# Optimization experiments

Hardware: AMD Instinct MI355X
Metric: run time of the kernel (lower is better)

## Reference

```python
import jax, jax.numpy as jnp
import numpy as np

A, B, O, C = 8, 32768, 256, 64   # num_agents, batch, obs_size, action_size
E, H = 128, 4                     # embedding_dim, attention_heads
Dh = E // H                       # attend_dim = 32
EPS = 1e-5                        # BatchNorm1d eps
SLOPE = 0.01                      # LeakyReLU default negative slope


def lrelu(x):
    return jnp.where(x >= 0, x, SLOPE * x)


def batchnorm(x, gamma, beta):
    # x: [A,B,F]; training-mode BatchNorm1d per agent (biased batch variance)
    mu = x.mean(axis=1, keepdims=True)
    var = x.var(axis=1, keepdims=True)
    return (x - mu) / jnp.sqrt(var + EPS) * gamma[:, None, :] + beta[:, None, :]


def setup_inputs() -> dict:
    key = jax.random.key(0)
    ks = jax.random.split(key, 13)
    s = lambda k, shape: jax.random.normal(k, shape, jnp.float32) * 0.05
    return {
        "observation_vector": jax.random.normal(ks[0], (A, B, O), jnp.float32),
        "action_vector": jax.random.normal(ks[1], (A, B, C), jnp.float32),
        "g_bn_gamma": jnp.ones((A, O + C), jnp.float32),
        "g_bn_beta": jnp.zeros((A, O + C), jnp.float32),
        "g_W": s(ks[2], (A, E, O + C)), "g_b": s(ks[3], (A, E)),
        "s_bn_gamma": jnp.ones((A, O), jnp.float32),
        "s_bn_beta": jnp.zeros((A, O), jnp.float32),
        "s_W": s(ks[4], (A, E, O)), "s_b": s(ks[5], (A, E)),
        "f_W1": s(ks[6], (A, E, 2 * E)), "f_b1": s(ks[7], (A, E)),
        "f_W2": s(ks[8], (A, C, E)), "f_b2": s(ks[9], (A, C)),
        "Wq": s(ks[10], (H, Dh, E)), "Wk": s(ks[11], (H, Dh, E)),
        "V": s(ks[12], (H, Dh, E)),
    }


def reference(observation_vector, action_vector, g_bn_gamma, g_bn_beta, g_W, g_b,
              s_bn_gamma, s_bn_beta, s_W, s_b, f_W1, f_b1, f_W2, f_b2, Wq, Wk, V):
    # per-agent embeddings of (obs, act) and obs-only
    combined = jnp.concatenate([observation_vector, action_vector], axis=2)      # [A,B,O+C]
    e = lrelu(jnp.einsum('abf,aef->abe', batchnorm(combined, g_bn_gamma, g_bn_beta), g_W)
              + g_b[:, None, :])                                                  # [A,B,E]
    si = lrelu(jnp.einsum('abf,aef->abe',
                          batchnorm(observation_vector, s_bn_gamma, s_bn_beta), s_W)
               + s_b[:, None, :])                                                 # [A,B,E]
    # NOTE: original applies F.softmax over a (batch,1) tensor -> every attention
    # weight is exactly 1.0, so x_i = sum_{j!=i} leaky_relu(V_l @ e_j). Wq/Wk only
    # feed the regularization logits (not returned when regularize=False).
    v = lrelu(jnp.einsum('abe,hde->abhd', e, V))                                  # [A,B,H,Dh]
    x = (v.sum(axis=0, keepdims=True) - v).reshape(A, B, E)                       # heads concatenated
    h = lrelu(jnp.einsum('abf,aef->abe', jnp.concatenate([x, si], axis=2), f_W1)
              + f_b1[:, None, :])                                                 # [A,B,E]
    q_all = jnp.einsum('abe,ace->abc', h, f_W2) + f_b2[:, None, :]                # [A,B,C]
    ids = jnp.argmax(action_vector, axis=2)[..., None]                            # [A,B,1]
    return jnp.take_along_axis(q_all, ids, axis=2)                                # [A,B,1]
```

## Files before the change

kernel.cpp:

```cpp
#include <hip/hip_runtime.h>
#include <hip/hip_bf16.h>
#include <stdint.h>

constexpr int A_ = 8, B_ = 32768, O_ = 256, C_ = 64, F_ = 320, E_ = 128;
constexpr int NCH = 128, CHROWS = B_ / NCH;
constexpr int NBT = B_ / 16;

typedef __attribute__((ext_vector_type(8))) __bf16 bf16x8;
typedef __attribute__((ext_vector_type(4))) float f32x4;
union U4 { uint4 u; bf16x8 v; __bf16 b[8]; };

__device__ __forceinline__ float lrelu(float x){ return x >= 0.f ? x : 0.01f*x; }
__device__ __forceinline__ f32x4 mfma16(bf16x8 a, bf16x8 b, f32x4 c){
  return __builtin_amdgcn_mfma_f32_16x16x32_bf16(a, b, c, 0, 0, 0);
}
__device__ __forceinline__ bf16x8 pk8(f32x4 lo, f32x4 hi){
  U4 r;
  r.b[0]=(__bf16)lo[0]; r.b[1]=(__bf16)lo[1]; r.b[2]=(__bf16)lo[2]; r.b[3]=(__bf16)lo[3];
  r.b[4]=(__bf16)hi[0]; r.b[5]=(__bf16)hi[1]; r.b[6]=(__bf16)hi[2]; r.b[7]=(__bf16)hi[3];
  return r.v;
}
__device__ __forceinline__ bf16x8 pk8f(float4 a, float4 b){
  U4 r;
  r.b[0]=(__bf16)a.x; r.b[1]=(__bf16)a.y; r.b[2]=(__bf16)a.z; r.b[3]=(__bf16)a.w;
  r.b[4]=(__bf16)b.x; r.b[5]=(__bf16)b.y; r.b[6]=(__bf16)b.z; r.b[7]=(__bf16)b.w;
  return r.v;
}
__device__ __forceinline__ void gl_lds16(const void* g, void* s){
  __builtin_amdgcn_global_load_lds(
      (const __attribute__((address_space(1))) unsigned int*)g,
      (__attribute__((address_space(3))) unsigned int*)s, 16, 0, 0);
}
template<int N> __device__ __forceinline__ void vmwait(){
  asm volatile("s_waitcnt vmcnt(%0)" :: "n"(N) : "memory");
}
__device__ __forceinline__ void lgkm0(){ asm volatile("s_waitcnt lgkmcnt(0)" ::: "memory"); }
__device__ __forceinline__ void sbar(){ __builtin_amdgcn_s_barrier(); }
__device__ __forceinline__ void schb(){ __builtin_amdgcn_sched_barrier(0); }

__global__ void k_stats_partial(const float* __restrict__ obs,
                                const float* __restrict__ act,
                                float* __restrict__ psum, float* __restrict__ psq,
                                int* __restrict__ ids){
  const int f = threadIdx.x, ch = blockIdx.x, a = blockIdx.y;
  const size_t b0 = (size_t)ch * CHROWS;
  float s = 0.f, q = 0.f;
  if (f < O_){
    const float* p = obs + ((size_t)a*B_ + b0)*O_ + f;
    for (int i = 0; i < CHROWS; ++i){ float x = p[(size_t)i*O_]; s += x; q += x*x; }
  } else {
    const float* p = act + ((size_t)a*B_ + b0)*C_ + (f - O_);
    for (int i = 0; i < CHROWS; ++i){ float x = p[(size_t)i*C_]; s += x; q += x*x; }
  }
  psum[((size_t)a*NCH + ch)*F_ + f] = s;
  psq [((size_t)a*NCH + ch)*F_ + f] = q;
  if (f < CHROWS){
    const float4* ar = (const float4*)(act + ((size_t)a*B_ + b0 + f)*C_);
    float best = -3.4e38f; int bi = 0;
    #pragma unroll 4
    for (int j = 0; j < 16; ++j){
      const float4 v = ar[j];
      const int c0 = j*4;
      if (v.x > best){ best = v.x; bi = c0;   }
      if (v.y > best){ best = v.y; bi = c0+1; }
      if (v.z > best){ best = v.z; bi = c0+2; }
      if (v.w > best){ best = v.w; bi = c0+3; }
    }
    ids[(size_t)a*B_ + b0 + f] = bi;
  }
}

__global__ void k_stats_final(const float* __restrict__ psum, const float* __restrict__ psq,
                              float* __restrict__ zscale, float* __restrict__ zshift){
  const int f = threadIdx.x, a = blockIdx.x;
  float s = 0.f, q = 0.f;
  for (int ch = 0; ch < NCH; ++ch){
    s += psum[((size_t)a*NCH + ch)*F_ + f];
    q += psq [((size_t)a*NCH + ch)*F_ + f];
  }
  const float mean = s * (1.0f / B_);
  float var = q * (1.0f / B_) - mean * mean;
  var = fmaxf(var, 0.0f);
  const float rs = rsqrtf(var + 1e-5f);
  zscale[a*F_ + f] = rs;
  zshift[a*F_ + f] = -mean * rs;
}

__global__ void k_prep_pack(const float* __restrict__ gW, const float* __restrict__ ggam,
                            const float* __restrict__ sW, const float* __restrict__ sgam,
                            const float* __restrict__ f1W, const float* __restrict__ f2W,
                            const float* __restrict__ Vm, const float* __restrict__ zscale,
                            __bf16* __restrict__ Ap, __bf16* __restrict__ Vp,
                            __bf16* __restrict__ B1p, __bf16* __restrict__ B2p){
  const int a = blockIdx.y;
  const int t0 = blockIdx.x*256 + threadIdx.x;
  constexpr int STR = 32*256;
  for (int i = t0; i < 10*16*64*8; i += STR){
    const int ks = i >> 13, mO = (i>>9)&15, l = (i>>3)&63, e = i&7;
    const int lg = l>>4, fo = mO*16 + (l&15), k = ks*32 + lg*8 + e;
    const float sc = zscale[a*F_ + k];
    float v;
    if (fo < 128) v = gW[(size_t)a*E_*F_ + (size_t)fo*F_ + k] * ggam[a*F_+k] * sc;
    else          v = (k < O_) ? sW[(size_t)a*E_*O_ + (size_t)(fo-128)*O_ + k] * sgam[a*O_+k] * sc : 0.f;
    Ap[(size_t)a*(10*16*64*8) + i] = (__bf16)v;
  }
  for (int i = t0; i < 8*8*64*8; i += STR){
    const int ks = i >> 12, mH = (i>>9)&7, l = (i>>3)&63, e = i&7;
    const int lg = l>>4, h = mH*16 + (l&15);
    const int f = 32*ks + 16*(e>>2) + 4*lg + (e&3);
    B1p[(size_t)a*(8*8*64*8) + i] = (__bf16)f1W[(size_t)a*E_*2*E_ + (size_t)h*2*E_ + f];
  }
  for (int i = t0; i < 4*4*64*8; i += STR){
    const int ks = i >> 11, mC = (i>>9)&3, l = (i>>3)&63, e = i&7;
    const int lg = l>>4, c = mC*16 + (l&15);
    const int f = 32*ks + 16*(e>>2) + 4*lg + (e&3);
    B2p[(size_t)a*(4*4*64*8) + i] = (__bf16)f2W[(size_t)a*C_*E_ + (size_t)c*E_ + f];
  }
  if (a == 0){
    for (int i = t0; i < 4*8*64*8; i += STR){
      const int ks = i >> 12, mV = (i>>9)&7, l = (i>>3)&63, e = i&7;
      const int lg = l>>4, vo = mV*16 + (l&15);
      const int f = 32*ks + 16*(e>>2) + 4*lg + (e&3);
      Vp[i] = (__bf16)Vm[(size_t)vo*E_ + f];
    }
  }
}

__global__ void k_prep_bias(const float* __restrict__ gW, const float* __restrict__ gb,
                            const float* __restrict__ ggam, const float* __restrict__ gbet,
                            const float* __restrict__ sW, const float* __restrict__ sb,
                            const float* __restrict__ sgam, const float* __restrict__ sbet,
                            const float* __restrict__ zshift, float* __restrict__ gsb){
  __shared__ float ww[F_];
  __shared__ float part[2][128];
  const int a = blockIdx.y, t = threadIdx.x;
  const int o = t & 127, h = t >> 7;
  if (blockIdx.x == 0){
    for (int f = t; f < F_; f += 256)
      ww[f] = gbet[a*F_+f] + ggam[a*F_+f]*zshift[a*F_+f];
    __syncthreads();
    float s = 0.f;
    #pragma unroll 4
    for (int f = h*160; f < h*160 + 160; f += 4){
      const float4 wv = *(const float4*)&gW[(size_t)a*E_*F_ + (size_t)o*F_ + f];
      s += wv.x*ww[f] + wv.y*ww[f+1] + wv.z*ww[f+2] + wv.w*ww[f+3];
    }
    part[h][o] = s;
    __syncthreads();
    if (t < 128) gsb[a*256 + t] = gb[a*E_+t] + part[0][t] + part[1][t];
  } else {
    for (int f = t; f < O_; f += 256)
      ww[f] = sbet[a*O_+f] + sgam[a*O_+f]*zshift[a*F_+f];
    __syncthreads();
    float s = 0.f;
    #pragma unroll 4
    for (int f = h*128; f < h*128 + 128; f += 4){
      const float4 wv = *(const float4*)&sW[(size_t)a*E_*O_ + (size_t)o*O_ + f];
      s += wv.x*ww[f] + wv.y*ww[f+1] + wv.z*ww[f+2] + wv.w*ww[f+3];
    }
    part[h][o] = s;
    __syncthreads();
    if (t < 128) gsb[a*256 + 128 + t] = sb[a*E_+t] + part[0][t] + part[1][t];
  }
}

__global__ __launch_bounds__(256, 2) void k_stageA(
    const float* __restrict__ obs, const float* __restrict__ act,
    const __bf16* __restrict__ Ap, const __bf16* __restrict__ Vp,
    const float* __restrict__ gsb,
    uint4* __restrict__ si_q, uint4* __restrict__ v_q){
  constexpr int BUF = 26624;
  __shared__ __align__(16) char smem[2*BUF];
  const int a = blockIdx.y, t = threadIdx.x;
  const int w = t>>6, l = t&63, l15 = l&15, lg = l>>4;
  const int bt0 = blockIdx.x*8;
  const size_t grow0 = (size_t)a*B_ + (size_t)bt0*16;
  const char* ApA = (const char*)Ap + (size_t)a*163840;
  const int xr = t>>1, kc0 = (t&1)*2;
  const float* obsrow = obs + (grow0 + xr)*O_;
  const float* actrow = act + (grow0 + xr)*C_;

  float4 xA[4], xB[4];

  auto wstage = [&](int ks, char* buf){
    const char* src = ApA + ks*16384;
    #pragma unroll
    for (int i = 0; i < 4; ++i)
      gl_lds16(src + (w*4+i)*1024 + l*16, buf + (w*4+i)*1024);
  };
  auto xload = [&](int ks, float4* d){
    const float* s = (ks < 8) ? (obsrow + ks*32 + kc0*8) : (actrow + (ks-8)*32 + kc0*8);
    d[0] = ((const float4*)s)[0]; d[1] = ((const float4*)s)[1];
    d[2] = ((const float4*)s)[2]; d[3] = ((const float4*)s)[3];
  };
  auto xwrite = [&](char* buf, const float4* d){
    *(bf16x8*)(buf + 16384 + xr*80 + kc0*16)     = pk8f(d[0], d[1]);
    *(bf16x8*)(buf + 16384 + xr*80 + (kc0+1)*16) = pk8f(d[2], d[3]);
  };

  f32x4 acc[4][8] = {};

  wstage(0, smem); schb();
  xload(0, xA);
  vmwait<0>();
  xwrite(smem, xA);
  xload(1, xB);
  lgkm0(); sbar(); schb();

  #pragma unroll
  for (int ks = 0; ks < 10; ++ks){
    char* cur = smem + (ks&1)*BUF;
    char* nxt = smem + ((ks+1)&1)*BUF;
    if (ks+1 < 10){ wstage(ks+1, nxt); schb(); }
    if (ks+2 < 10) xload(ks+2, (ks&1) ? xB : xA);
    {
      const bf16x8* wc = (const bf16x8*)cur;
      const char* xb = cur + 16384;
      bf16x8 bfr[8];
      #pragma unroll
      for (int nt = 0; nt < 8; ++nt)
        bfr[nt] = *(const bf16x8*)(xb + (nt*16 + l15)*80 + lg*16);
      #pragma unroll
      for (int m = 0; m < 4; ++m){
        const bf16x8 af = wc[(w*4+m)*64 + l];
        #pragma unroll
        for (int nt = 0; nt < 8; ++nt)
          acc[m][nt] = mfma16(af, bfr[nt], acc[m][nt]);
      }
    }
    schb();
    if (ks <= 7)      vmwait<4>();
    else if (ks == 8) vmwait<0>();
    if (ks+1 < 10) xwrite(nxt, (ks&1) ? xA : xB);
    if (ks < 9){ lgkm0(); sbar(); schb(); }
  }

  const float* bE = gsb + a*256 + w*64 + lg*4;
  #pragma unroll
  for (int m = 0; m < 4; ++m){
    const float4 b = *(const float4*)(bE + m*16);
    #pragma unroll
    for (int nt = 0; nt < 8; ++nt){
      acc[m][nt][0] = lrelu(acc[m][nt][0] + b.x);
      acc[m][nt][1] = lrelu(acc[m][nt][1] + b.y);
      acc[m][nt][2] = lrelu(acc[m][nt][2] + b.z);
      acc[m][nt][3] = lrelu(acc[m][nt][3] + b.w);
    }
  }
  sbar();

  if (w < 2){
    #pragma unroll
    for (int jp = 0; jp < 2; ++jp){
      const int kv = 2*w + jp;
      #pragma unroll
      for (int nt = 0; nt < 8; ++nt)
        *(bf16x8*)(smem + ((kv*8 + nt)*64 + l)*16) = pk8(acc[2*jp][nt], acc[2*jp+1][nt]);
    }
  } else {
    #pragma unroll
    for (int jp = 0; jp < 2; ++jp){
      const int j = 2*(w-2) + jp;
      #pragma unroll
      for (int nt = 0; nt < 8; ++nt){
        U4 u; u.v = pk8(acc[2*jp][nt], acc[2*jp+1][nt]);
        si_q[(((size_t)a*NBT + bt0 + nt)*4 + j)*64 + l] = u.u;
      }
    }
  }
  lgkm0(); sbar(); schb();

  const uint4* Vq = (const uint4*)Vp;
  f32x4 accv[2][8] = {};
  #pragma unroll
  for (int kv = 0; kv < 4; ++kv){
    U4 a0, a1;
    a0.u = Vq[(kv*8 + w*2 + 0)*64 + l];
    a1.u = Vq[(kv*8 + w*2 + 1)*64 + l];
    bf16x8 bv[8];
    #pragma unroll
    for (int nt = 0; nt < 8; ++nt)
      bv[nt] = *(const bf16x8*)(smem + ((kv*8 + nt)*64 + l)*16);
    #pragma unroll
    for (int nt = 0; nt < 8; ++nt){
      accv[0][nt] = mfma16(a0.v, bv[nt], accv[0][nt]);
      accv[1][nt] = mfma16(a1.v, bv[nt], accv[1][nt]);
    }
  }
  #pragma unroll
  for (int nt = 0; nt < 8; ++nt){
    f32x4 lo, hi;
    #pragma unroll
    for (int e = 0; e < 4; ++e){ lo[e] = lrelu(accv[0][nt][e]); hi[e] = lrelu(accv[1][nt][e]); }
    U4 u; u.v = pk8(lo, hi);
    v_q[(((size_t)a*NBT + bt0 + nt)*4 + w)*64 + l] = u.u;
  }
}

__global__ void k_vsum(const uint4* __restrict__ v_q, uint4* __restrict__ vsum_q){
  const size_t i = (size_t)blockIdx.x*256 + threadIdx.x;
  const size_t per_a = (size_t)NBT*4*64;
  float s[8] = {0,0,0,0,0,0,0,0};
  #pragma unroll
  for (int aa = 0; aa < 8; ++aa){
    U4 u; u.u = v_q[aa*per_a + i];
    #pragma unroll
    for (int e = 0; e < 8; ++e) s[e] += (float)u.b[e];
  }
  U4 o;
  #pragma unroll
  for (int e = 0; e < 8; ++e) o.b[e] = (__bf16)s[e];
  vsum_q[i] = o.u;
}

__global__ __launch_bounds__(256, 2) void k_stageC(
    const uint4* __restrict__ v_q, const uint4* __restrict__ si_q,
    const uint4* __restrict__ vsum_q,
    const __bf16* __restrict__ B1p, const __bf16* __restrict__ B2p,
    const float* __restrict__ f1b, const float* __restrict__ f2b,
    const int* __restrict__ ids, float* __restrict__ out){
  __shared__ __align__(16) char wsm[2*8192];
  __shared__ float qs[4][64][17];
  const int a = blockIdx.y, t = threadIdx.x;
  const int w = t>>6, l = t&63, l15 = l&15, lg = l>>4;
  const int btw = blockIdx.x*16 + w*4;
  const char* B1A = (const char*)B1p + (size_t)a*65536;
  const size_t vbase = (size_t)a*NBT*4*64;

  uint4 qA[4], qB[4], sA[4], sB[4];

  auto wstage = [&](int ks, char* dst){
    const char* src = B1A + ks*8192;
    #pragma unroll
    for (int i = 0; i < 2; ++i)
      gl_lds16(src + (w*2+i)*1024 + l*16, dst + (w*2+i)*1024);
  };
  auto bload = [&](int ks, uint4* qv, uint4* sv){
    if (ks < 4){
      #pragma unroll
      for (int nt = 0; nt < 4; ++nt){
        const size_t idx = ((size_t)(btw+nt)*4 + ks)*64 + l;
        qv[nt] = v_q[vbase + idx];
        sv[nt] = vsum_q[idx];
      }
    } else {
      #pragma unroll
      for (int nt = 0; nt < 4; ++nt)
        qv[nt] = si_q[vbase + ((size_t)(btw+nt)*4 + (ks-4))*64 + l];
    }
  };
  auto bmake = [&](int ks, const uint4* qv, const uint4* sv, bf16x8* bf){
    if (ks < 4){
      #pragma unroll
      for (int nt = 0; nt < 4; ++nt){
        U4 s, v; s.u = sv[nt]; v.u = qv[nt];
        f32x4 lo, hi;
        #pragma unroll
        for (int e = 0; e < 4; ++e){
          lo[e] = (float)s.b[e]   - (float)v.b[e];
          hi[e] = (float)s.b[e+4] - (float)v.b[e+4];
        }
        bf[nt] = pk8(lo, hi);
      }
    } else {
      #pragma unroll
      for (int nt = 0; nt < 4; ++nt){ U4 u; u.u = qv[nt]; bf[nt] = u.v; }
    }
  };

  f32x4 hacc[8][4] = {};
  wstage(0, wsm); schb();
  bload(0, qA, sA); schb();
  bload(1, qB, sB);
  vmwait<8>();
  sbar(); schb();

  #pragma unroll
  for (int ks = 0; ks < 8; ++ks){
    bf16x8 bf[4];
    bmake(ks, (ks&1) ? qB : qA, (ks&1) ? sB : sA, bf);
    if (ks+1 < 8){ wstage(ks+1, wsm + ((ks+1)&1)*8192); schb(); }
    if (ks+2 < 8) bload(ks+2, (ks&1) ? qB : qA, (ks&1) ? sB : sA);
    {
      const bf16x8* wc = (const bf16x8*)(wsm + (ks&1)*8192);
      #pragma unroll
      for (int m = 0; m < 8; ++m){
        const bf16x8 af = wc[m*64 + l];
        #pragma unroll
        for (int nt = 0; nt < 4; ++nt)
          hacc[m][nt] = mfma16(af, bf[nt], hacc[m][nt]);
      }
    }
    schb();
    if (ks <= 1)      vmwait<8>();
    else if (ks <= 5) vmwait<4>();
    else if (ks == 6) vmwait<0>();
    if (ks < 7){ sbar(); schb(); }
  }

  bf16x8 hb[4][4];
  const float* bH = f1b + a*E_ + lg*4;
  #pragma unroll
  for (int kq = 0; kq < 4; ++kq){
    const float4 b0v = *(const float4*)(bH + (2*kq)*16);
    const float4 b1v = *(const float4*)(bH + (2*kq+1)*16);
    #pragma unroll
    for (int nt = 0; nt < 4; ++nt){
      f32x4 lo, hi;
      lo[0]=lrelu(hacc[2*kq][nt][0]+b0v.x); lo[1]=lrelu(hacc[2*kq][nt][1]+b0v.y);
      lo[2]=lrelu(hacc[2*kq][nt][2]+b0v.z); lo[3]=lrelu(hacc[2*kq][nt][3]+b0v.w);
      hi[0]=lrelu(hacc[2*kq+1][nt][0]+b1v.x); hi[1]=lrelu(hacc[2*kq+1][nt][1]+b1v.y);
      hi[2]=lrelu(hacc[2*kq+1][nt][2]+b1v.z); hi[3]=lrelu(hacc[2*kq+1][nt][3]+b1v.w);
      hb[kq][nt] = pk8(lo, hi);
    }
  }
  const uint4* A2q = (const uint4*)(B2p + (size_t)a*(4*4*64*8));
  f32x4 accq[4][4] = {};
  #pragma unroll
  for (int kq = 0; kq < 4; ++kq){
    #pragma unroll
    for (int mC = 0; mC < 4; ++mC){
      U4 af; af.u = A2q[(kq*4 + mC)*64 + l];
      #pragma unroll
      for (int nt = 0; nt < 4; ++nt)
        accq[mC][nt] = mfma16(af.v, hb[kq][nt], accq[mC][nt]);
    }
  }
  const float* bQ = f2b + a*C_ + lg*4;
  float4 qb[4];
  #pragma unroll
  for (int mC = 0; mC < 4; ++mC) qb[mC] = *(const float4*)(bQ + mC*16);
  #pragma unroll
  for (int nt = 0; nt < 4; ++nt){
    #pragma unroll
    for (int mC = 0; mC < 4; ++mC){
      qs[w][mC*16 + lg*4 + 0][l15] = accq[mC][nt][0] + qb[mC].x;
      qs[w][mC*16 + lg*4 + 1][l15] = accq[mC][nt][1] + qb[mC].y;
      qs[w][mC*16 + lg*4 + 2][l15] = accq[mC][nt][2] + qb[mC].z;
      qs[w][mC*16 + lg*4 + 3][l15] = accq[mC][nt][3] + qb[mC].w;
    }
    lgkm0();
    if (l < 16){
      const size_t row = (size_t)(btw + nt)*16 + l;
      const int id = ids[(size_t)a*B_ + row];
      out[(size_t)a*B_ + row] = qs[w][id][l];
    }
    lgkm0();
  }
}

extern "C" void kernel_launch(void* const* d_in, const int* in_sizes, int n_in,
                              void* d_out, int out_size, void* d_ws, size_t ws_size,
                              hipStream_t stream) {
  const float* obs  = (const float*)d_in[0];
  const float* act  = (const float*)d_in[1];
  const float* ggam = (const float*)d_in[2];
  const float* gbet = (const float*)d_in[3];
  const float* gW   = (const float*)d_in[4];
  const float* gb   = (const float*)d_in[5];
  const float* sgam = (const float*)d_in[6];
  const float* sbet = (const float*)d_in[7];
  const float* sW   = (const float*)d_in[8];
  const float* sb   = (const float*)d_in[9];
  const float* f1W  = (const float*)d_in[10];
  const float* f1b  = (const float*)d_in[11];
  const float* f2W  = (const float*)d_in[12];
  const float* f2b  = (const float*)d_in[13];
  const float* Vm   = (const float*)d_in[16];
  float* out = (float*)d_out;

  char* base = (char*)d_ws; size_t off = 0;
  auto alloc = [&](size_t bytes) -> void* {
    off = (off + 255) & ~(size_t)255; void* p = base + off; off += bytes; return p;
  };
  float* psum    = (float*)alloc((size_t)A_*NCH*F_*4);
  float* psq     = (float*)alloc((size_t)A_*NCH*F_*4);
  float* zscale  = (float*)alloc((size_t)A_*F_*4);
  float* zshift  = (float*)alloc((size_t)A_*F_*4);
  float* gsb     = (float*)alloc((size_t)A_*256*4);
  __bf16* Ap     = (__bf16*)alloc((size_t)A_*10*16*64*8*2);
  __bf16* Vp     = (__bf16*)alloc((size_t)4*8*64*8*2);
  __bf16* B1p    = (__bf16*)alloc((size_t)A_*8*8*64*8*2);
  __bf16* B2p    = (__bf16*)alloc((size_t)A_*4*4*64*8*2);
  uint4* si_q    = (uint4*)alloc((size_t)A_*NBT*4*64*16);
  uint4* v_q     = (uint4*)alloc((size_t)A_*NBT*4*64*16);
  uint4* vsum_q  = (uint4*)alloc((size_t)NBT*4*64*16);
  int*   ids     = (int*)alloc((size_t)A_*B_*4);
  (void)ws_size; (void)in_sizes; (void)n_in; (void)out_size;

  k_stats_partial<<<dim3(NCH, A_), 320, 0, stream>>>(obs, act, psum, psq, ids);
  k_stats_final<<<A_, F_, 0, stream>>>(psum, psq, zscale, zshift);
  k_prep_pack<<<dim3(32, A_), 256, 0, stream>>>(gW, ggam, sW, sgam, f1W, f2W, Vm,
                                                zscale, Ap, Vp, B1p, B2p);
  k_prep_bias<<<dim3(2, A_), 256, 0, stream>>>(gW, gb, ggam, gbet, sW, sb, sgam, sbet,
                                               zshift, gsb);
  k_stageA<<<dim3(NBT/8, A_), 256, 0, stream>>>(obs, act, Ap, Vp, gsb, si_q, v_q);
  k_vsum<<<(NBT*4*64)/256, 256, 0, stream>>>(v_q, vsum_q);
  k_stageC<<<dim3(NBT/16, A_), 256, 0, stream>>>(v_q, si_q, vsum_q, B1p, B2p,
                                                 f1b, f2b, ids, out);
}
```

Before: 271.1 us.

## Pre-pack inputs to bf16 during stats pass and stream packed tiles into stageA

The statistics kernel now reads obs/act once in row tiles, computes per-column partial sums through shared memory, computes argmax ids, and writes a swizzled bf16 copy of the inputs in MFMA-ready layout. StageA then loads this half-size packed tensor directly into LDS through a three-deep global_load_lds ring. Weights are held in registers, double-buffered. This removes stageA's second fp32 read of the inputs and its in-kernel conversion. The cost is an extra bf16 write and read of the packed activations, plus more partial-sum blocks for the final reduction.

```diff
diff --git a/kernel.cpp b/kernel.cpp
--- a/kernel.cpp
+++ b/kernel.cpp
@@ -3,7 +3,7 @@
 #include <stdint.h>
 
 constexpr int A_ = 8, B_ = 32768, O_ = 256, C_ = 64, F_ = 320, E_ = 128;
-constexpr int NCH = 128, CHROWS = B_ / NCH;
+constexpr int NRB = B_ / 128;
 constexpr int NBT = B_ / 16;
 
 typedef __attribute__((ext_vector_type(8))) __bf16 bf16x8;
@@ -38,35 +38,68 @@
 __device__ __forceinline__ void sbar(){ __builtin_amdgcn_s_barrier(); }
 __device__ __forceinline__ void schb(){ __builtin_amdgcn_sched_barrier(0); }
 
-__global__ void k_stats_partial(const float* __restrict__ obs,
-                                const float* __restrict__ act,
-                                float* __restrict__ psum, float* __restrict__ psq,
-                                int* __restrict__ ids){
-  const int f = threadIdx.x, ch = blockIdx.x, a = blockIdx.y;
-  const size_t b0 = (size_t)ch * CHROWS;
-  float s = 0.f, q = 0.f;
-  if (f < O_){
-    const float* p = obs + ((size_t)a*B_ + b0)*O_ + f;
-    for (int i = 0; i < CHROWS; ++i){ float x = p[(size_t)i*O_]; s += x; q += x*x; }
-  } else {
-    const float* p = act + ((size_t)a*B_ + b0)*C_ + (f - O_);
-    for (int i = 0; i < CHROWS; ++i){ float x = p[(size_t)i*C_]; s += x; q += x*x; }
-  }
-  psum[((size_t)a*NCH + ch)*F_ + f] = s;
-  psq [((size_t)a*NCH + ch)*F_ + f] = q;
-  if (f < CHROWS){
-    const float4* ar = (const float4*)(act + ((size_t)a*B_ + b0 + f)*C_);
-    float best = -3.4e38f; int bi = 0;
+__global__ __launch_bounds__(256) void k_xstats(
+    const float* __restrict__ obs, const float* __restrict__ act,
+    __bf16* __restrict__ xpk, float* __restrict__ psum, float* __restrict__ psq,
+    int* __restrict__ ids){
+  __shared__ float tile[128*36];
+  __shared__ float sred[32][9], qred[32][9];
+  const int a = blockIdx.y, rb = blockIdx.x, t = threadIdx.x;
+  const int r = t >> 1, fh = t & 1;
+  const size_t row0 = (size_t)a*B_ + (size_t)rb*128;
+  float abest = -3.4e38f; int abi = 0;
+
+  for (int c = 0; c < 10; ++c){
+    const float* src = (c < 8) ? obs + (row0 + r)*O_ + c*32 + fh*16
+                               : act + (row0 + r)*C_ + (c-8)*32 + fh*16;
+    const float4 v0 = ((const float4*)src)[0];
+    const float4 v1 = ((const float4*)src)[1];
+    const float4 v2 = ((const float4*)src)[2];
+    const float4 v3 = ((const float4*)src)[3];
+    if (c >= 8){
+      const int fb = (c-8)*32 + fh*16;
+      const float4 vv[4] = {v0, v1, v2, v3};
+      #pragma unroll
+      for (int j = 0; j < 4; ++j){
+        if (vv[j].x > abest){ abest = vv[j].x; abi = fb + j*4;   }
+        if (vv[j].y > abest){ abest = vv[j].y; abi = fb + j*4+1; }
+        if (vv[j].z > abest){ abest = vv[j].z; abi = fb + j*4+2; }
+        if (vv[j].w > abest){ abest = vv[j].w; abi = fb + j*4+3; }
+      }
+    }
+    const int u = r >> 1, swz = u & 7;
+    const int j0 = ((r&1)*4 + fh*2    ) ^ swz;
+    const int j1 = ((r&1)*4 + fh*2 + 1) ^ swz;
+    bf16x8* xb = (bf16x8*)xpk + ((size_t)(a*NRB + rb)*10 + c)*512 + u*8;
+    xb[j0] = pk8f(v0, v1);
+    xb[j1] = pk8f(v2, v3);
+    float* tr = tile + r*36 + fh*16;
+    *(float4*)(tr)    = v0; *(float4*)(tr+4)  = v1;
+    *(float4*)(tr+8)  = v2; *(float4*)(tr+12) = v3;
+    __syncthreads();
+    const int f = t & 31, g = t >> 5;
+    float s = 0.f, q = 0.f;
     #pragma unroll 4
-    for (int j = 0; j < 16; ++j){
-      const float4 v = ar[j];
-      const int c0 = j*4;
-      if (v.x > best){ best = v.x; bi = c0;   }
-      if (v.y > best){ best = v.y; bi = c0+1; }
-      if (v.z > best){ best = v.z; bi = c0+2; }
-      if (v.w > best){ best = v.w; bi = c0+3; }
-    }
-    ids[(size_t)a*B_ + b0 + f] = bi;
+    for (int i = 0; i < 16; ++i){
+      const float x = tile[(g*16+i)*36 + f];
+      s += x; q += x*x;
+    }
+    sred[f][g] = s; qred[f][g] = q;
+    __syncthreads();
+    if (t < 32){
+      float ss = 0.f, qq = 0.f;
+      #pragma unroll
+      for (int g2 = 0; g2 < 8; ++g2){ ss += sred[t][g2]; qq += qred[t][g2]; }
+      psum[((size_t)a*NRB + rb)*F_ + c*32 + t] = ss;
+      psq [((size_t)a*NRB + rb)*F_ + c*32 + t] = qq;
+    }
+    __syncthreads();
+  }
+  {
+    const float ob = __shfl_xor(abest, 1, 64);
+    const int   oi = __shfl_xor(abi,   1, 64);
+    if (ob > abest || (ob == abest && oi < abi)){ abest = ob; abi = oi; }
+    if (fh == 0) ids[row0 + r] = abi;
   }
 }
 
@@ -74,9 +107,9 @@
                               float* __restrict__ zscale, float* __restrict__ zshift){
   const int f = threadIdx.x, a = blockIdx.x;
   float s = 0.f, q = 0.f;
-  for (int ch = 0; ch < NCH; ++ch){
-    s += psum[((size_t)a*NCH + ch)*F_ + f];
-    q += psq [((size_t)a*NCH + ch)*F_ + f];
+  for (int rb = 0; rb < NRB; ++rb){
+    s += psum[((size_t)a*NRB + rb)*F_ + f];
+    q += psq [((size_t)a*NRB + rb)*F_ + f];
   }
   const float mean = s * (1.0f / B_);
   float var = q * (1.0f / B_) - mean * mean;
@@ -164,75 +197,59 @@
   }
 }
 
-__global__ __launch_bounds__(256, 2) void k_stageA(
-    const float* __restrict__ obs, const float* __restrict__ act,
+__global__ __launch_bounds__(256) void k_stageA(
+    const __bf16* __restrict__ xpk,
     const __bf16* __restrict__ Ap, const __bf16* __restrict__ Vp,
     const float* __restrict__ gsb,
     uint4* __restrict__ si_q, uint4* __restrict__ v_q){
-  constexpr int BUF = 26624;
-  __shared__ __align__(16) char smem[2*BUF];
+  __shared__ __align__(16) char smem[32768];
   const int a = blockIdx.y, t = threadIdx.x;
   const int w = t>>6, l = t&63, l15 = l&15, lg = l>>4;
-  const int bt0 = blockIdx.x*8;
-  const size_t grow0 = (size_t)a*B_ + (size_t)bt0*16;
+  const int rb = blockIdx.x;
+  const int bt0 = rb*8;
+  const char* xT  = (const char*)xpk + ((size_t)(a*NRB + rb))*81920;
   const char* ApA = (const char*)Ap + (size_t)a*163840;
-  const int xr = t>>1, kc0 = (t&1)*2;
-  const float* obsrow = obs + (grow0 + xr)*O_;
-  const float* actrow = act + (grow0 + xr)*C_;
-
-  float4 xA[4], xB[4];
-
-  auto wstage = [&](int ks, char* buf){
-    const char* src = ApA + ks*16384;
-    #pragma unroll
-    for (int i = 0; i < 4; ++i)
-      gl_lds16(src + (w*4+i)*1024 + l*16, buf + (w*4+i)*1024);
+  const int xcj = (((l15&1)<<2) | lg) ^ ((l15>>1)&7);
+  const int xbase = (l15>>1)*128 + xcj*16;
+
+  U4 wA[2][4];
+  auto wload = [&](int ks){
+    const uint4* p = (const uint4*)(ApA + ks*16384) + w*256 + l;
+    U4* d = wA[ks&1];
+    d[0].u = p[0]; d[1].u = p[64]; d[2].u = p[128]; d[3].u = p[192];
   };
-  auto xload = [&](int ks, float4* d){
-    const float* s = (ks < 8) ? (obsrow + ks*32 + kc0*8) : (actrow + (ks-8)*32 + kc0*8);
-    d[0] = ((const float4*)s)[0]; d[1] = ((const float4*)s)[1];
-    d[2] = ((const float4*)s)[2]; d[3] = ((const float4*)s)[3];
+  auto xstage = [&](int ks){
+    const char* s = xT + ks*8192;
+    char* d = smem + (ks%3)*8192;
+    gl_lds16(s + ((w*2+0)*64+l)*16, d + (w*2+0)*1024);
+    gl_lds16(s + ((w*2+1)*64+l)*16, d + (w*2+1)*1024);
   };
-  auto xwrite = [&](char* buf, const float4* d){
-    *(bf16x8*)(buf + 16384 + xr*80 + kc0*16)     = pk8f(d[0], d[1]);
-    *(bf16x8*)(buf + 16384 + xr*80 + (kc0+1)*16) = pk8f(d[2], d[3]);
-  };
 
   f32x4 acc[4][8] = {};
-
-  wstage(0, smem); schb();
-  xload(0, xA);
-  vmwait<0>();
-  xwrite(smem, xA);
-  xload(1, xB);
-  lgkm0(); sbar(); schb();
+  wload(0); schb();
+  xstage(0); xstage(1); schb();
+  vmwait<2>(); sbar(); schb();
 
   #pragma unroll
   for (int ks = 0; ks < 10; ++ks){
-    char* cur = smem + (ks&1)*BUF;
-    char* nxt = smem + ((ks+1)&1)*BUF;
-    if (ks+1 < 10){ wstage(ks+1, nxt); schb(); }
-    if (ks+2 < 10) xload(ks+2, (ks&1) ? xB : xA);
-    {
-      const bf16x8* wc = (const bf16x8*)cur;
-      const char* xb = cur + 16384;
-      bf16x8 bfr[8];
+    if (ks+1 < 10){ wload(ks+1); schb(); }
+    if (ks+2 < 10){ xstage(ks+2); schb(); }
+    const char* xb = smem + (ks%3)*8192;
+    bf16x8 bfr[8];
+    #pragma unroll
+    for (int nt = 0; nt < 8; ++nt)
+      bfr[nt] = *(const bf16x8*)(xb + nt*1024 + xbase);
+    #pragma unroll
+    for (int m = 0; m < 4; ++m){
+      const bf16x8 af = wA[ks&1][m].v;
       #pragma unroll
       for (int nt = 0; nt < 8; ++nt)
-        bfr[nt] = *(const bf16x8*)(xb + (nt*16 + l15)*80 + lg*16);
-      #pragma unroll
-      for (int m = 0; m < 4; ++m){
-        const bf16x8 af = wc[(w*4+m)*64 + l];
-        #pragma unroll
-        for (int nt = 0; nt < 8; ++nt)
-          acc[m][nt] = mfma16(af, bfr[nt], acc[m][nt]);
-      }
+        acc[m][nt] = mfma16(af, bfr[nt], acc[m][nt]);
     }
     schb();
-    if (ks <= 7)      vmwait<4>();
+    if (ks < 8)       vmwait<2>();
     else if (ks == 8) vmwait<0>();
-    if (ks+1 < 10) xwrite(nxt, (ks&1) ? xA : xB);
-    if (ks < 9){ lgkm0(); sbar(); schb(); }
+    if (ks < 9){ sbar(); schb(); }
   }
 
   const float* bE = gsb + a*256 + w*64 + lg*4;
@@ -473,11 +490,12 @@
   auto alloc = [&](size_t bytes) -> void* {
     off = (off + 255) & ~(size_t)255; void* p = base + off; off += bytes; return p;
   };
-  float* psum    = (float*)alloc((size_t)A_*NCH*F_*4);
-  float* psq     = (float*)alloc((size_t)A_*NCH*F_*4);
+  float* psum    = (float*)alloc((size_t)A_*NRB*F_*4);
+  float* psq     = (float*)alloc((size_t)A_*NRB*F_*4);
   float* zscale  = (float*)alloc((size_t)A_*F_*4);
   float* zshift  = (float*)alloc((size_t)A_*F_*4);
   float* gsb     = (float*)alloc((size_t)A_*256*4);
+  __bf16* xpk    = (__bf16*)alloc((size_t)A_*NRB*10*512*16);
   __bf16* Ap     = (__bf16*)alloc((size_t)A_*10*16*64*8*2);
   __bf16* Vp     = (__bf16*)alloc((size_t)4*8*64*8*2);
   __bf16* B1p    = (__bf16*)alloc((size_t)A_*8*8*64*8*2);
@@ -488,13 +506,13 @@
   int*   ids     = (int*)alloc((size_t)A_*B_*4);
   (void)ws_size; (void)in_sizes; (void)n_in; (void)out_size;
 
-  k_stats_partial<<<dim3(NCH, A_), 320, 0, stream>>>(obs, act, psum, psq, ids);
+  k_xstats<<<dim3(NRB, A_), 256, 0, stream>>>(obs, act, xpk, psum, psq, ids);
   k_stats_final<<<A_, F_, 0, stream>>>(psum, psq, zscale, zshift);
   k_prep_pack<<<dim3(32, A_), 256, 0, stream>>>(gW, ggam, sW, sgam, f1W, f2W, Vm,
                                                 zscale, Ap, Vp, B1p, B2p);
   k_prep_bias<<<dim3(2, A_), 256, 0, stream>>>(gW, gb, ggam, gbet, sW, sb, sgam, sbet,
                                                zshift, gsb);
-  k_stageA<<<dim3(NBT/8, A_), 256, 0, stream>>>(obs, act, Ap, Vp, gsb, si_q, v_q);
+  k_stageA<<<dim3(NRB, A_), 256, 0, stream>>>(xpk, Ap, Vp, gsb, si_q, v_q);
   k_vsum<<<(NBT*4*64)/256, 256, 0, stream>>>(v_q, vsum_q);
   k_stageC<<<dim3(NBT/16, A_), 256, 0, stream>>>(v_q, si_q, vsum_q, B1p, B2p,
                                                  f1b, f2b, ids, out);
```

Result: slower. 327.3 us (+20.8%).
